# Kernel tuning notes

Measured on AMD Instinct MI355X. Metric: run time of the kernel, lower is better.

The kernel has to match this reference:

```python
import jax, jax.numpy as jnp
import numpy as np

B, L, D = 2, 2048, 2048
H, KVH, Dh = 16, 8, 128
S_ROPE = 1024
EPS = 1e-5


def rms_norm(x, w):
    xf = x.astype(jnp.float32)
    xf = xf * jax.lax.rsqrt(jnp.mean(xf * xf, axis=-1, keepdims=True) + EPS)
    return (xf * w).astype(x.dtype)


def rotate_half(x):
    x1, x2 = jnp.split(x, 2, axis=-1)
    return jnp.concatenate((-x2, x1), axis=-1)


def setup_inputs() -> dict:
    key = jax.random.key(0)
    ks = jax.random.split(key, 12)
    sc = 0.02
    # 1D rope tables at every absolute position (theta = 500000 as in config)
    inv_freq = 1.0 / (500000.0 ** (np.arange(0, Dh, 2, dtype=np.float32) / Dh))
    ang = np.arange(L, dtype=np.float32)[:, None] * inv_freq[None, :]  # [L, Dh/2]
    emb = np.concatenate([ang, ang], axis=-1)  # [L, Dh]
    # 3D rope as per-pair 2x2 rotation matrices
    ang3 = np.random.RandomState(0).uniform(-np.pi, np.pi, size=(S_ROPE, Dh // 2)).astype(np.float32)
    R = np.stack([np.stack([np.cos(ang3), -np.sin(ang3)], -1),
                  np.stack([np.sin(ang3), np.cos(ang3)], -1)], -2)  # [S,Dh/2,2,2]
    mpos = jnp.array([[[128, 1025], [1160, 513]],
                      [[128, 1025], [1160, 513]]], dtype=jnp.int64)
    return {
        "hidden_states": jax.random.normal(ks[0], (B, L, D), jnp.float32),
        "temb": jax.random.normal(ks[1], (B, D), jnp.float32),
        "w_ln": jnp.ones((D,), jnp.float32),
        "w_mod": jax.random.normal(ks[2], (D, 3 * D), jnp.float32) * sc,
        "b_mod": jnp.zeros((3 * D,), jnp.float32),
        "wq": jax.random.normal(ks[3], (D, H * Dh), jnp.float32) * sc,
        "wk": jax.random.normal(ks[4], (D, KVH * Dh), jnp.float32) * sc,
        "wv": jax.random.normal(ks[5], (D, KVH * Dh), jnp.float32) * sc,
        "wo": jax.random.normal(ks[6], (H * Dh, D), jnp.float32) * sc,
        "qn_w": jnp.ones((Dh,), jnp.float32),
        "kn_w": jnp.ones((Dh,), jnp.float32),
        "cos_1d": jnp.asarray(np.cos(emb)),
        "sin_1d": jnp.asarray(np.sin(emb)),
        "rope_3d": jnp.asarray(R),
        "modality_positions": mpos,
    }


def _masks(modality_positions):
    pos = jnp.arange(L)  # [L]
    off = modality_positions[..., 0]   # [B, S]
    ln = modality_positions[..., 1]    # [B, S]
    meta = 1  # add_time_embeds=True, add_ar_embeds=False
    seg_end = off + jnp.maximum(ln, meta)
    in_full = (pos[None, None, :] >= off[..., None]) & (pos[None, None, :] < seg_end[..., None])
    text_mask = ~jnp.any(in_full, axis=1)  # [B, L]
    img_start = off + meta
    in_img = (pos[None, None, :] >= img_start[..., None]) & (pos[None, None, :] < (off + ln)[..., None])
    rel = jnp.sum(jnp.where(in_img, pos[None, None, :] - img_start[..., None], 0), axis=1)  # [B, L]
    img_mask = jnp.any(in_img, axis=1) & (rel < S_ROPE) & (rel >= 0)
    rel = jnp.clip(rel, 0, S_ROPE - 1)
    return text_mask, img_mask, rel


def _apply_mixed_rope(q, k, cos_1d, sin_1d, rope_3d, text_mask, img_mask, rel):
    # text 1D rope (rotate_half style), applied at absolute position
    c = cos_1d[None, None]  # [1,1,L,Dh]
    s = sin_1d[None, None]
    q_txt = q * c + rotate_half(q) * s
    k_txt = k * c + rotate_half(k) * s
    # image 3D rope: per-pair 2x2 rotation gathered at within-image index
    R = rope_3d[rel]  # [B, L, Dh/2, 2, 2]
    q2 = q.reshape(*q.shape[:-1], Dh // 2, 2)
    k2 = k.reshape(*k.shape[:-1], Dh // 2, 2)
    q_img = jnp.einsum('bhlpi,blpij->bhlpj', q2, R).reshape(q.shape)
    k_img = jnp.einsum('bhlpi,blpij->bhlpj', k2, R).reshape(k.shape)
    mt = text_mask[:, None, :, None]
    mi = img_mask[:, None, :, None]
    q_out = jnp.where(mt, q_txt, jnp.where(mi, q_img, q))
    k_out = jnp.where(mt, k_txt, jnp.where(mi, k_img, k))
    return q_out, k_out


def reference(hidden_states, temb, w_ln, w_mod, b_mod, wq, wk, wv, wo,
              qn_w, kn_w, cos_1d, sin_1d, rope_3d, modality_positions):
    dtype = hidden_states.dtype
    # adaLN modulation
    mod = jax.nn.silu(temb) @ w_mod + b_mod  # [B, 3D]
    shift, scale, gate = jnp.split(mod, 3, axis=-1)
    xn = rms_norm(hidden_states, w_ln)
    xm = (xn.astype(jnp.float32) * (1.0 + scale[:, None, :].astype(jnp.float32))
          + shift[:, None, :].astype(jnp.float32)).astype(dtype)
    # qkv projections (GQA)
    q = (xm @ wq).reshape(B, L, H, Dh).transpose(0, 2, 1, 3)
    k = (xm @ wk).reshape(B, L, KVH, Dh).transpose(0, 2, 1, 3)
    v = (xm @ wv).reshape(B, L, KVH, Dh).transpose(0, 2, 1, 3)
    # qk-norm over head_dim
    q = rms_norm(q, qn_w)
    k = rms_norm(k, kn_w)
    # mixed 3D-image / 1D-text RoPE
    text_mask, img_mask, rel = _masks(modality_positions)
    q, k = _apply_mixed_rope(q, k, cos_1d, sin_1d, rope_3d, text_mask, img_mask, rel)
    # GQA: repeat kv heads (repeat_interleave along head dim)
    n_rep = H // KVH
    k = jnp.repeat(k, n_rep, axis=1)
    v = jnp.repeat(v, n_rep, axis=1)
    # full attention (no causal mask for diffusion block)
    scores = jnp.einsum('bhqd,bhkd->bhqk', q, k) / jnp.sqrt(jnp.asarray(Dh, q.dtype))
    attn = jax.nn.softmax(scores, axis=-1)
    o = jnp.einsum('bhqk,bhkd->bhqd', attn, v)
    o = o.transpose(0, 2, 1, 3).reshape(B, L, H * Dh) @ wo
    return hidden_states + gate[:, None, :].astype(dtype) * o


if __name__ == '__main__':
    out = reference(**setup_inputs())
    print(out.shape, out.dtype)
```

## Files before the change

### kernel.cpp

```cpp
#include <hip/hip_runtime.h>
#include <hip/hip_bf16.h>
#include <stdint.h>
#include <math.h>

typedef unsigned short u16;
typedef __attribute__((ext_vector_type(8))) short short8;
typedef __attribute__((ext_vector_type(4))) float fx4;
typedef __attribute__((ext_vector_type(4))) unsigned short u16x4;

#define DEV __device__ __forceinline__

DEV u16 f2bf(float f) {
  return __builtin_bit_cast(u16, __float2bfloat16(f));
}
DEV float bf2f(u16 h) { return __builtin_bit_cast(float, ((unsigned)h) << 16); }

DEV fx4 mfma16(short8 a, short8 b, fx4 c) {
  return __builtin_amdgcn_mfma_f32_16x16x32_bf16(a, b, c, 0, 0, 0);
}

#if __has_builtin(__builtin_amdgcn_exp2f)
DEV float exp2v(float x) { return __builtin_amdgcn_exp2f(x); }
#else
DEV float exp2v(float x) { return exp2f(x); }
#endif

#define GLD16(g, l)                                                            \
  __builtin_amdgcn_global_load_lds(                                            \
      (const __attribute__((address_space(1))) void*)(g),                      \
      (__attribute__((address_space(3))) void*)(l), 16, 0, 0)

#define WAIT_ALL() asm volatile("s_waitcnt vmcnt(0) lgkmcnt(0)" ::: "memory")
#define WAIT_VM4() asm volatile("s_waitcnt vmcnt(4)" ::: "memory")
#define WAIT_VM0() asm volatile("s_waitcnt vmcnt(0)" ::: "memory")

__global__ __launch_bounds__(512) void k_pre(
    const float* __restrict__ temb, const float* __restrict__ wmod,
    const float* __restrict__ bmod, float* __restrict__ mod,
    const float* __restrict__ wq, const float* __restrict__ wk,
    const float* __restrict__ wv, u16* __restrict__ wT) {
  __shared__ float st[4096];
  __shared__ float red[8][2][64];
  __shared__ float t2[2][32][33];
  int bid = blockIdx.x;
  int tid = threadIdx.x;
  if (bid < 96) {
    for (int i = tid; i < 4096; i += 512) {
      float t = temb[i];
      st[i] = t / (1.0f + __expf(-t));
    }
    __syncthreads();
    int j = bid * 64 + (tid & 63);
    int ks = tid >> 6;
    float a0 = 0.f, a1 = 0.f;
    for (int d = ks * 256; d < ks * 256 + 256; ++d) {
      float w = wmod[(size_t)d * 6144 + j];
      a0 += st[d] * w;
      a1 += st[2048 + d] * w;
    }
    red[ks][0][tid & 63] = a0;
    red[ks][1][tid & 63] = a1;
    __syncthreads();
    if (tid < 64) {
      float s0 = 0.f, s1 = 0.f;
#pragma unroll
      for (int i = 0; i < 8; ++i) {
        s0 += red[i][0][tid];
        s1 += red[i][1][tid];
      }
      mod[j] = s0 + bmod[j];
      mod[6144 + j] = s1 + bmod[j];
    }
  } else {
    int half = tid >> 8;
    int sub = tid & 255;
    int tx = sub & 31, ty = sub >> 5;
    int tt = (bid - 96) * 2 + half;
    const float* src;
    u16* dst;
    int cols, kb, nb;
    if (tt < 4096) {
      src = wq; dst = wT; cols = 2048;
      kb = (tt & 63) * 32; nb = (tt >> 6) * 32;
    } else if (tt < 6144) {
      int u = tt - 4096;
      src = wk; dst = wT + (size_t)2048 * 2048; cols = 1024;
      kb = (u & 63) * 32; nb = (u >> 6) * 32;
    } else {
      int u = tt - 6144;
      src = wv; dst = wT + (size_t)3072 * 2048; cols = 1024;
      kb = (u & 63) * 32; nb = (u >> 6) * 32;
    }
    float (*t)[33] = t2[half];
#pragma unroll
    for (int i = 0; i < 4; ++i)
      t[ty + i * 8][tx] = src[(size_t)(kb + ty + i * 8) * cols + nb + tx];
    __syncthreads();
    int nl = ty * 4 + (tx >> 3);
    int k4 = (tx & 7) * 4;
    u16x4 v;
#pragma unroll
    for (int j = 0; j < 4; ++j) v[j] = f2bf(t[k4 + j][nl]);
    *(u16x4*)(dst + (size_t)(nb + nl) * 2048 + kb + k4) = v;
  }
}

__global__ __launch_bounds__(256) void k_xm(
    const float* __restrict__ x, const float* __restrict__ wln,
    const float* __restrict__ mod, u16* __restrict__ xm) {
  int row = blockIdx.x;
  int b = row >> 11;
  const float* xr = x + (size_t)row * 2048;
  int tid = threadIdx.x;
  float4 v0 = ((const float4*)xr)[tid];
  float4 v1 = ((const float4*)xr)[tid + 256];
  float ss = v0.x * v0.x + v0.y * v0.y + v0.z * v0.z + v0.w * v0.w +
             v1.x * v1.x + v1.y * v1.y + v1.z * v1.z + v1.w * v1.w;
  for (int m = 1; m < 64; m <<= 1) ss += __shfl_xor(ss, m);
  __shared__ float red[4];
  if ((tid & 63) == 0) red[tid >> 6] = ss;
  __syncthreads();
  ss = red[0] + red[1] + red[2] + red[3];
  float r = rsqrtf(ss * (1.0f / 2048.0f) + 1e-5f);
  const float* mb = mod + (size_t)b * 6144;
#pragma unroll
  for (int c = 0; c < 2; ++c) {
    int j0 = (tid + c * 256) * 4;
    float4 xv = c ? v1 : v0;
    float4 sh = *(const float4*)(mb + j0);
    float4 sc = *(const float4*)(mb + 2048 + j0);
    float4 wl = *(const float4*)(wln + j0);
    u16x4 o;
    o.x = f2bf(xv.x * r * wl.x * (1.f + sc.x) + sh.x);
    o.y = f2bf(xv.y * r * wl.y * (1.f + sc.y) + sh.y);
    o.z = f2bf(xv.z * r * wl.z * (1.f + sc.z) + sh.z);
    o.w = f2bf(xv.w * r * wl.w * (1.f + sc.w) + sh.w);
    *(u16x4*)(xm + (size_t)row * 2048 + j0) = o;
  }
}

__global__ __launch_bounds__(512, 1) void k_gemm256(
    const u16* __restrict__ A, const u16* __restrict__ Bt, u16* __restrict__ C,
    int N, int K) {
  __shared__ u16 As[3][256 * 32];
  __shared__ u16 Bs[3][256 * 32];
  int tid = threadIdx.x;
  int wave = tid >> 6, lane = tid & 63, quad = lane >> 4, l16 = lane & 15;
  int gx = gridDim.x;
  int nwg = gx * gridDim.y;
  int lin = blockIdx.y * gx + blockIdx.x;
  int cpx = nwg >> 3;
  int swz = (lin & 7) * cpx + (lin >> 3);
  int m0 = (swz / gx) * 256, n0 = (swz % gx) * 256;
  int wm = (wave >> 2) * 128, wn = (wave & 3) * 64;
  fx4 acc[8][4] = {};
  int rowa = tid >> 2;
  int chunk = (tid & 3) ^ ((rowa >> 1) & 3);
  int cola = chunk * 8;
  const u16* Ag = A + (size_t)(m0 + rowa) * K + cola;
  const u16* Bg = Bt + (size_t)(n0 + rowa) * K + cola;
  int sl = (quad ^ ((l16 >> 1) & 3)) * 8;

  auto STAGE = [&](int k0, int buf) {
    u16* AsW = &As[buf][wave * 512];
    u16* BsW = &Bs[buf][wave * 512];
    GLD16(Ag + k0, AsW);
    GLD16(Ag + k0 + (size_t)128 * K, AsW + 4096);
    GLD16(Bg + k0, BsW);
    GLD16(Bg + k0 + (size_t)128 * K, BsW + 4096);
  };
  auto COMPUTE = [&](int buf) {
    short8 af[8], bfr[4];
#pragma unroll
    for (int i = 0; i < 8; ++i)
      af[i] = *(const short8*)&As[buf][(wm + i * 16 + l16) * 32 + sl];
#pragma unroll
    for (int j = 0; j < 4; ++j)
      bfr[j] = *(const short8*)&Bs[buf][(wn + j * 16 + l16) * 32 + sl];
#pragma unroll
    for (int i = 0; i < 8; ++i)
#pragma unroll
      for (int j = 0; j < 4; ++j) acc[i][j] = mfma16(af[i], bfr[j], acc[i][j]);
  };

  STAGE(0, 0);
  STAGE(32, 1);
  for (int t = 0; t < 62; ++t) {
    WAIT_VM4();
    __builtin_amdgcn_s_barrier();
    STAGE((t + 2) * 32, (t + 2) % 3);
    COMPUTE(t % 3);
  }
  WAIT_VM4();
  __builtin_amdgcn_s_barrier();
  COMPUTE(2);
  WAIT_VM0();
  __builtin_amdgcn_s_barrier();
  COMPUTE(0);

#pragma unroll
  for (int i = 0; i < 8; ++i) {
    int row = m0 + wm + i * 16 + quad * 4;
#pragma unroll
    for (int j = 0; j < 4; ++j) {
      int col = n0 + wn + j * 16 + l16;
#pragma unroll
      for (int r = 0; r < 4; ++r)
        C[(size_t)(row + r) * N + col] = f2bf(acc[i][j][r]);
    }
  }
}

__global__ __launch_bounds__(256) void k_mid(
    const float* __restrict__ wo, u16* __restrict__ woT,
    const u16* __restrict__ qkv, const float* __restrict__ qn,
    const float* __restrict__ kn, const float* __restrict__ cos1,
    const float* __restrict__ sin1, const float* __restrict__ r3,
    const int* __restrict__ mpos, u16* __restrict__ Q, u16* __restrict__ Kb,
    u16* __restrict__ VT) {
  __shared__ float tc[32][33];
  __shared__ u16 tv[64][65];
  int bid = blockIdx.x;
  int tid = threadIdx.x;
  if (bid < 4096) {
    int kb = (bid & 63) * 32, nb = (bid >> 6) * 32;
    int tx = tid & 31, ty = tid >> 5;
#pragma unroll
    for (int i = 0; i < 4; ++i)
      tc[ty + i * 8][tx] = wo[(size_t)(kb + ty + i * 8) * 2048 + nb + tx];
    __syncthreads();
    int nl = ty * 4 + (tx >> 3);
    int k4 = (tx & 7) * 4;
    u16x4 v;
#pragma unroll
    for (int j = 0; j < 4; ++j) v[j] = f2bf(tc[k4 + j][nl]);
    *(u16x4*)(woT + (size_t)(nb + nl) * 2048 + kb + k4) = v;
  } else if (bid < 8192) {
    int bx = bid - 4096;
    int b = bx >> 11, l = bx & 2047;
    int slot = tid >> 3, sub = tid & 7;
    if (slot >= 24) return;
    bool isq = slot < 16;
    int head = isq ? slot : slot - 16;
    const u16* base =
        qkv + (size_t)bx * 4096 + (isq ? slot * 128 : 2048 + head * 128);
    int d0 = sub * 16;
    short8 sx0 = *(const short8*)(base + d0);
    short8 sx1 = *(const short8*)(base + d0 + 8);
    float xv[16];
#pragma unroll
    for (int i = 0; i < 8; ++i) {
      xv[i] = bf2f((u16)sx0[i]);
      xv[8 + i] = bf2f((u16)sx1[i]);
    }
    float ss = 0.f;
#pragma unroll
    for (int i = 0; i < 16; ++i) ss += xv[i] * xv[i];
    ss += __shfl_xor(ss, 1);
    ss += __shfl_xor(ss, 2);
    ss += __shfl_xor(ss, 4);
    float r = rsqrtf(ss * (1.0f / 128.0f) + 1e-5f);
    int mp[8];
    {
      bool is64 =
          (mpos[1] == 0) & (mpos[3] == 0) & (mpos[5] == 0) & (mpos[7] == 0);
#pragma unroll
      for (int i = 0; i < 8; ++i) mp[i] = is64 ? mpos[2 * i] : mpos[i];
    }
    bool infull = false, inimg = false;
    int rel = 0;
#pragma unroll
    for (int s = 0; s < 2; ++s) {
      int off = mp[b * 4 + s * 2], ln = mp[b * 4 + s * 2 + 1];
      int mx = ln > 1 ? ln : 1;
      infull |= (l >= off) && (l < off + mx);
      bool ii = (l >= off + 1) && (l < off + ln);
      inimg |= ii;
      rel += ii ? (l - (off + 1)) : 0;
    }
    bool text = !infull;
    bool img = inimg && (rel < 1024);
    const float* w = isq ? qn : kn;
    fx4 wv4[4];
#pragma unroll
    for (int q = 0; q < 4; ++q) wv4[q] = *(const fx4*)(w + d0 + q * 4);
    float out[16];
    if (text) {
      int dp0 = d0 ^ 64;
      float sgn = (d0 < 64) ? -1.f : 1.f;
      short8 sp0 = *(const short8*)(base + dp0);
      short8 sp1 = *(const short8*)(base + dp0 + 8);
      fx4 cv[4], sv[4], wp[4];
#pragma unroll
      for (int q = 0; q < 4; ++q) {
        cv[q] = *(const fx4*)(cos1 + (size_t)l * 128 + d0 + q * 4);
        sv[q] = *(const fx4*)(sin1 + (size_t)l * 128 + d0 + q * 4);
        wp[q] = *(const fx4*)(w + dp0 + q * 4);
      }
#pragma unroll
      for (int i = 0; i < 16; ++i) {
        float xp = bf2f((u16)(i < 8 ? sp0[i & 7] : sp1[i & 7]));
        out[i] = r * (xv[i] * wv4[i >> 2][i & 3] * cv[i >> 2][i & 3] +
                      sgn * xp * wp[i >> 2][i & 3] * sv[i >> 2][i & 3]);
      }
    } else if (img) {
      const fx4* Rv = (const fx4*)(r3 + ((size_t)rel * 64 + (d0 >> 1)) * 4);
#pragma unroll
      for (int p = 0; p < 8; ++p) {
        fx4 R = Rv[p];
        float a = xv[2 * p] * wv4[(2 * p) >> 2][(2 * p) & 3] * r;
        float c2 = xv[2 * p + 1] * wv4[(2 * p + 1) >> 2][(2 * p + 1) & 3] * r;
        out[2 * p] = a * R[0] + c2 * R[2];
        out[2 * p + 1] = a * R[1] + c2 * R[3];
      }
    } else {
#pragma unroll
      for (int i = 0; i < 16; ++i) out[i] = xv[i] * wv4[i >> 2][i & 3] * r;
    }
    float qs = isq ? (0.08838834764831845f * 1.4426950408889634f) : 1.0f;
    short8 o0, o1;
#pragma unroll
    for (int i = 0; i < 8; ++i) {
      o0[i] = (short)f2bf(out[i] * qs);
      o1[i] = (short)f2bf(out[8 + i] * qs);
    }
    u16* dst = isq ? (Q + ((size_t)(b * 16 + head) * 2048 + l) * 128 + d0)
                   : (Kb + ((size_t)(b * 8 + head) * 2048 + l) * 128 + d0);
    *(short8*)dst = o0;
    *(short8*)(dst + 8) = o1;
  } else {
    int v = bid - 8192;
    int bh = v & 15;
    int l0 = ((v >> 4) & 31) * 64, d0 = (v >> 9) * 64;
    int b = bh >> 3, kvh = bh & 7;
    int lr = tid >> 4;
    int c4 = (tid & 15) * 4;
#pragma unroll
    for (int i = 0; i < 4; ++i) {
      int li = lr + i * 16;
      *(u16x4*)&tv[li][c4] = *(const u16x4*)(
          qkv + (size_t)(b * 2048 + l0 + li) * 4096 + 3072 + kvh * 128 + d0 + c4);
    }
    __syncthreads();
#pragma unroll
    for (int i = 0; i < 4; ++i) {
      int di = lr + i * 16;
      u16x4 vv;
      vv[0] = tv[c4 + 0][di];
      vv[1] = tv[c4 + 1][di];
      vv[2] = tv[c4 + 2][di];
      vv[3] = tv[c4 + 3][di];
      *(u16x4*)(VT + ((size_t)bh * 128 + d0 + di) * 2048 + l0 + c4) = vv;
    }
  }
}

__global__ __launch_bounds__(512, 4) void k_attn(
    const u16* __restrict__ Q, const u16* __restrict__ Kb,
    const u16* __restrict__ VT, u16* __restrict__ O) {
  __shared__ u16 Ks[2][64 * 128];
  __shared__ u16 Vs[2][128 * 64];
  __shared__ u16 Ps[128 * 64];
  int tid = threadIdx.x;
  int wave = tid >> 6, lane = tid & 63, quad = lane >> 4, l16 = lane & 15;
  int lin = blockIdx.y * gridDim.x + blockIdx.x;
  int vb = (lin & 7) * 64 + (lin >> 3);
  int q0 = (vb & 15) * 128;
  int bh = vb >> 4;
  int b = bh >> 4, h = bh & 15, kvh = h >> 1;
  const u16* Qb = Q + ((size_t)bh * 2048 + q0 + wave * 16) * 128;
  short8 qf[4];
#pragma unroll
  for (int ks = 0; ks < 4; ++ks)
    qf[ks] = *(const short8*)(Qb + l16 * 128 + ks * 32 + quad * 8);
  const u16* Kg = Kb + (size_t)(b * 8 + kvh) * 2048 * 128;
  const u16* Vg = VT + (size_t)(b * 8 + kvh) * 128 * 2048;
  float mrow[4], lpart[4];
  fx4 of[8] = {};
#pragma unroll
  for (int r = 0; r < 4; ++r) {
    mrow[r] = -INFINITY;
    lpart[r] = 0.f;
  }
  size_t kgo[2], vgo[2];
#pragma unroll
  for (int i = 0; i < 2; ++i) {
    int kr = i * 32 + wave * 4 + (lane >> 4);
    kgo[i] = (size_t)kr * 128 + (((lane & 15) ^ (kr & 15)) * 8);
    int vr = i * 64 + wave * 8 + (lane >> 3);
    vgo[i] = (size_t)vr * 2048 + (((lane & 7) ^ (vr & 7)) * 8);
  }

  auto STAGE = [&](int t, int buf) {
    size_t ko = (size_t)t * 8192;
    size_t vo = (size_t)t * 64;
#pragma unroll
    for (int i = 0; i < 2; ++i) {
      GLD16(Kg + ko + kgo[i], &Ks[buf][i * 4096 + wave * 512]);
      GLD16(Vg + vo + vgo[i], &Vs[buf][i * 4096 + wave * 512]);
    }
  };

  auto COMPUTE = [&](int buf) {
    fx4 sf[4] = {};
    __builtin_amdgcn_s_setprio(1);
#pragma unroll
    for (int ct = 0; ct < 4; ++ct) {
#pragma unroll
      for (int ks = 0; ks < 4; ++ks) {
        short8 kf = *(const short8*)&Ks[buf][(ct * 16 + l16) * 128 +
                                            (((ks * 4 + quad) ^ l16) * 8)];
        sf[ct] = mfma16(qf[ks], kf, sf[ct]);
      }
    }
    __builtin_amdgcn_s_setprio(0);
    float cmv[4];
    bool need = false;
#pragma unroll
    for (int r = 0; r < 4; ++r) {
      cmv[r] = fmaxf(fmaxf(sf[0][r], sf[1][r]), fmaxf(sf[2][r], sf[3][r]));
      need |= (cmv[r] > mrow[r] + 8.0f);
    }
    if (__any(need)) {
#pragma unroll
      for (int r = 0; r < 4; ++r) {
        float cm = cmv[r];
        cm = fmaxf(cm, __shfl_xor(cm, 1));
        cm = fmaxf(cm, __shfl_xor(cm, 2));
        cm = fmaxf(cm, __shfl_xor(cm, 4));
        cm = fmaxf(cm, __shfl_xor(cm, 8));
        float mn = fmaxf(mrow[r], cm);
        float al = exp2v(mrow[r] - mn);
        mrow[r] = mn;
        lpart[r] *= al;
#pragma unroll
        for (int c2 = 0; c2 < 8; ++c2) of[c2][r] *= al;
      }
    }
    int hb = l16 >> 3;
#pragma unroll
    for (int r = 0; r < 4; ++r) {
      float p0 = exp2v(sf[0][r] - mrow[r]);
      float p1 = exp2v(sf[1][r] - mrow[r]);
      float p2 = exp2v(sf[2][r] - mrow[r]);
      float p3 = exp2v(sf[3][r] - mrow[r]);
      lpart[r] += (p0 + p1) + (p2 + p3);
      int prow = wave * 16 + quad * 4 + r;
      int pb = prow * 64, px = prow & 7, lo = l16 & 7;
      Ps[pb + ((0 + hb) ^ px) * 8 + lo] = f2bf(p0);
      Ps[pb + ((2 + hb) ^ px) * 8 + lo] = f2bf(p1);
      Ps[pb + ((4 + hb) ^ px) * 8 + lo] = f2bf(p2);
      Ps[pb + ((6 + hb) ^ px) * 8 + lo] = f2bf(p3);
    }
    __builtin_amdgcn_s_setprio(1);
#pragma unroll
    for (int ks2 = 0; ks2 < 2; ++ks2) {
      int rsl = (((ks2 * 4 + quad) ^ (l16 & 7)) * 8);
      short8 pa = *(const short8*)&Ps[(wave * 16 + l16) * 64 + rsl];
#pragma unroll
      for (int c2 = 0; c2 < 8; ++c2) {
        short8 vb2 = *(const short8*)&Vs[buf][(c2 * 16 + l16) * 64 + rsl];
        of[c2] = mfma16(pa, vb2, of[c2]);
      }
    }
    __builtin_amdgcn_s_setprio(0);
  };

  STAGE(0, 0);
  WAIT_ALL();
  __builtin_amdgcn_s_barrier();
  int cur = 0;
  for (int t = 0; t < 31; ++t) {
    STAGE(t + 1, cur ^ 1);
    COMPUTE(cur);
    WAIT_ALL();
    __builtin_amdgcn_s_barrier();
    cur ^= 1;
  }
  COMPUTE(cur);

#pragma unroll
  for (int r = 0; r < 4; ++r) {
    float ls = lpart[r];
    ls += __shfl_xor(ls, 1);
    ls += __shfl_xor(ls, 2);
    ls += __shfl_xor(ls, 4);
    ls += __shfl_xor(ls, 8);
    float inv = 1.0f / ls;
    int qrow = q0 + wave * 16 + quad * 4 + r;
#pragma unroll
    for (int c2 = 0; c2 < 8; ++c2)
      O[((size_t)b * 2048 + qrow) * 2048 + h * 128 + c2 * 16 + l16] =
          f2bf(of[c2][r] * inv);
  }
}

__global__ __launch_bounds__(256) void k_gemm(
    const u16* __restrict__ A, const u16* __restrict__ Bt, float* __restrict__ C,
    const float* __restrict__ hid, const float* __restrict__ mod, int N, int K) {
  __shared__ u16 As[3][128 * 32];
  __shared__ u16 Bs[3][128 * 32];
  int tid = threadIdx.x;
  int wave = tid >> 6, lane = tid & 63, quad = lane >> 4, l16 = lane & 15;
  int gx = gridDim.x;
  int nwg = gx * gridDim.y;
  int lin = blockIdx.y * gx + blockIdx.x;
  int cpx = nwg >> 3;
  int swz = (lin & 7) * cpx + (lin >> 3);
  int m0 = (swz / gx) * 128, n0 = (swz % gx) * 128;
  int wm = (wave >> 1) * 64, wn = (wave & 1) * 64;
  fx4 acc[4][4] = {};
  int rowa = tid >> 2;
  int chunk = (tid & 3) ^ ((rowa >> 1) & 3);
  int cola = chunk * 8;
  const u16* Ag = A + (size_t)(m0 + rowa) * K + cola;
  const u16* Bg = Bt + (size_t)(n0 + rowa) * K + cola;
  int sl = (quad ^ ((l16 >> 1) & 3)) * 8;

  auto STAGE = [&](int k0, int buf) {
    u16* AsW = &As[buf][wave * 512];
    u16* BsW = &Bs[buf][wave * 512];
    GLD16(Ag + k0, AsW);
    GLD16(Ag + k0 + (size_t)64 * K, AsW + 2048);
    GLD16(Bg + k0, BsW);
    GLD16(Bg + k0 + (size_t)64 * K, BsW + 2048);
  };
  auto COMPUTE = [&](int buf) {
    short8 af[4], bfr[4];
#pragma unroll
    for (int i = 0; i < 4; ++i) {
      af[i] = *(const short8*)&As[buf][(wm + i * 16 + l16) * 32 + sl];
      bfr[i] = *(const short8*)&Bs[buf][(wn + i * 16 + l16) * 32 + sl];
    }
#pragma unroll
    for (int i = 0; i < 4; ++i)
#pragma unroll
      for (int j = 0; j < 4; ++j) acc[i][j] = mfma16(af[i], bfr[j], acc[i][j]);
  };

  STAGE(0, 0);
  STAGE(32, 1);
  int nk = K >> 5;
  for (int t = 0; t < nk - 2; ++t) {
    WAIT_VM4();
    __builtin_amdgcn_s_barrier();
    STAGE((t + 2) * 32, (t + 2) % 3);
    COMPUTE(t % 3);
  }
  WAIT_VM4();
  __builtin_amdgcn_s_barrier();
  COMPUTE((nk - 2) % 3);
  WAIT_VM0();
  __builtin_amdgcn_s_barrier();
  COMPUTE((nk - 1) % 3);

#pragma unroll
  for (int i = 0; i < 4; ++i) {
    int row = m0 + wm + i * 16 + quad * 4;
#pragma unroll
    for (int j = 0; j < 4; ++j) {
      int col = n0 + wn + j * 16 + l16;
      int b = row >> 11;
      float g = mod[(size_t)b * 6144 + 4096 + col];
#pragma unroll
      for (int r = 0; r < 4; ++r)
        C[(size_t)(row + r) * N + col] =
            hid[(size_t)(row + r) * N + col] + g * acc[i][j][r];
    }
  }
}

extern "C" void kernel_launch(void* const* d_in, const int* in_sizes, int n_in,
                              void* d_out, int out_size, void* d_ws, size_t ws_size,
                              hipStream_t stream) {
  (void)in_sizes; (void)n_in; (void)out_size; (void)ws_size;
  const float* hid  = (const float*)d_in[0];
  const float* temb = (const float*)d_in[1];
  const float* wln  = (const float*)d_in[2];
  const float* wmod = (const float*)d_in[3];
  const float* bmod = (const float*)d_in[4];
  const float* wq   = (const float*)d_in[5];
  const float* wk   = (const float*)d_in[6];
  const float* wv   = (const float*)d_in[7];
  const float* wo   = (const float*)d_in[8];
  const float* qn   = (const float*)d_in[9];
  const float* kn   = (const float*)d_in[10];
  const float* cos1 = (const float*)d_in[11];
  const float* sin1 = (const float*)d_in[12];
  const float* r3   = (const float*)d_in[13];
  const int*   mpos = (const int*)d_in[14];

  char* ws = (char*)d_ws;
  float* mod = (float*)(ws + 0);
  u16* xm  = (u16*)(ws + 49152);
  u16* wT  = (u16*)(ws + 16826368);
  u16* woT = wT;
  u16* qkv = (u16*)(ws + 33603584);
  u16* Qb  = (u16*)(ws + 67158016);
  u16* Kv  = (u16*)(ws + 83935232);
  u16* VT  = (u16*)(ws + 92323840);
  u16* Ob  = qkv;

  k_pre<<<4192, 512, 0, stream>>>(temb, wmod, bmod, mod, wq, wk, wv, wT);
  k_xm<<<4096, 256, 0, stream>>>(hid, wln, mod, xm);
  k_gemm256<<<dim3(16, 16), 512, 0, stream>>>(xm, wT, qkv, 4096, 2048);
  k_mid<<<9216, 256, 0, stream>>>(wo, woT, qkv, qn, kn, cos1, sin1, r3, mpos,
                                  Qb, Kv, VT);
  k_attn<<<dim3(16, 32), 512, 0, stream>>>(Qb, Kv, VT, Ob);
  k_gemm<<<dim3(16, 32), 256, 0, stream>>>(Ob, woT, (float*)d_out, hid, mod,
                                           2048, 2048);
}
```

Baseline: 461.2 us.

## Process two query tiles per wave in attention to reuse K/V fragments

Each attention workgroup now handles 256 query rows, and each wave computes two 16-row query tiles against the same K and V fragments loaded from LDS. This halves K/V staging and LDS fragment reads per query row and doubles MFMA work per load. In exchange, the accumulator registers and P-buffer LDS double, the occupancy hint drops to 2, and the grid shrinks to 256 workgroups, which may under-fill the GPU's compute units.

```diff
diff --git a/kernel.cpp b/kernel.cpp
--- a/kernel.cpp
+++ b/kernel.cpp
@@ -355,33 +355,38 @@
   }
 }
 
-__global__ __launch_bounds__(512, 4) void k_attn(
+__global__ __launch_bounds__(512, 2) void k_attn(
     const u16* __restrict__ Q, const u16* __restrict__ Kb,
     const u16* __restrict__ VT, u16* __restrict__ O) {
   __shared__ u16 Ks[2][64 * 128];
   __shared__ u16 Vs[2][128 * 64];
-  __shared__ u16 Ps[128 * 64];
+  __shared__ u16 Ps[256 * 64];
   int tid = threadIdx.x;
   int wave = tid >> 6, lane = tid & 63, quad = lane >> 4, l16 = lane & 15;
   int lin = blockIdx.y * gridDim.x + blockIdx.x;
-  int vb = (lin & 7) * 64 + (lin >> 3);
-  int q0 = (vb & 15) * 128;
-  int bh = vb >> 4;
+  int vb = (lin & 7) * 32 + (lin >> 3);
+  int q0 = (vb & 7) * 256;
+  int bh = vb >> 3;
   int b = bh >> 4, h = bh & 15, kvh = h >> 1;
   const u16* Qb = Q + ((size_t)bh * 2048 + q0 + wave * 16) * 128;
-  short8 qf[4];
-#pragma unroll
-  for (int ks = 0; ks < 4; ++ks)
-    qf[ks] = *(const short8*)(Qb + l16 * 128 + ks * 32 + quad * 8);
+  short8 qf[2][4];
+#pragma unroll
+  for (int qt = 0; qt < 2; ++qt)
+#pragma unroll
+    for (int ks = 0; ks < 4; ++ks)
+      qf[qt][ks] =
+          *(const short8*)(Qb + ((size_t)qt * 128 + l16) * 128 + ks * 32 + quad * 8);
   const u16* Kg = Kb + (size_t)(b * 8 + kvh) * 2048 * 128;
   const u16* Vg = VT + (size_t)(b * 8 + kvh) * 128 * 2048;
-  float mrow[4], lpart[4];
-  fx4 of[8] = {};
-#pragma unroll
-  for (int r = 0; r < 4; ++r) {
-    mrow[r] = -INFINITY;
-    lpart[r] = 0.f;
-  }
+  float mrow[2][4], lpart[2][4];
+  fx4 of[2][8] = {};
+#pragma unroll
+  for (int qt = 0; qt < 2; ++qt)
+#pragma unroll
+    for (int r = 0; r < 4; ++r) {
+      mrow[qt][r] = -INFINITY;
+      lpart[qt][r] = 0.f;
+    }
   size_t kgo[2], vgo[2];
 #pragma unroll
   for (int i = 0; i < 2; ++i) {
@@ -402,7 +407,7 @@
   };
 
   auto COMPUTE = [&](int buf) {
-    fx4 sf[4] = {};
+    fx4 sf[2][4] = {};
     __builtin_amdgcn_s_setprio(1);
 #pragma unroll
     for (int ct = 0; ct < 4; ++ct) {
@@ -410,57 +415,67 @@
       for (int ks = 0; ks < 4; ++ks) {
         short8 kf = *(const short8*)&Ks[buf][(ct * 16 + l16) * 128 +
                                             (((ks * 4 + quad) ^ l16) * 8)];
-        sf[ct] = mfma16(qf[ks], kf, sf[ct]);
+        sf[0][ct] = mfma16(qf[0][ks], kf, sf[0][ct]);
+        sf[1][ct] = mfma16(qf[1][ks], kf, sf[1][ct]);
       }
     }
     __builtin_amdgcn_s_setprio(0);
-    float cmv[4];
+    float cmv[2][4];
     bool need = false;
 #pragma unroll
-    for (int r = 0; r < 4; ++r) {
-      cmv[r] = fmaxf(fmaxf(sf[0][r], sf[1][r]), fmaxf(sf[2][r], sf[3][r]));
-      need |= (cmv[r] > mrow[r] + 8.0f);
-    }
+    for (int qt = 0; qt < 2; ++qt)
+#pragma unroll
+      for (int r = 0; r < 4; ++r) {
+        cmv[qt][r] = fmaxf(fmaxf(sf[qt][0][r], sf[qt][1][r]),
+                           fmaxf(sf[qt][2][r], sf[qt][3][r]));
+        need |= (cmv[qt][r] > mrow[qt][r] + 8.0f);
+      }
     if (__any(need)) {
 #pragma unroll
+      for (int qt = 0; qt < 2; ++qt)
+#pragma unroll
+        for (int r = 0; r < 4; ++r) {
+          float cm = cmv[qt][r];
+          cm = fmaxf(cm, __shfl_xor(cm, 1));
+          cm = fmaxf(cm, __shfl_xor(cm, 2));
+          cm = fmaxf(cm, __shfl_xor(cm, 4));
+          cm = fmaxf(cm, __shfl_xor(cm, 8));
+          float mn = fmaxf(mrow[qt][r], cm);
+          float al = exp2v(mrow[qt][r] - mn);
+          mrow[qt][r] = mn;
+          lpart[qt][r] *= al;
+#pragma unroll
+          for (int c2 = 0; c2 < 8; ++c2) of[qt][c2][r] *= al;
+        }
+    }
+    int hb = l16 >> 3;
+#pragma unroll
+    for (int qt = 0; qt < 2; ++qt)
+#pragma unroll
       for (int r = 0; r < 4; ++r) {
-        float cm = cmv[r];
-        cm = fmaxf(cm, __shfl_xor(cm, 1));
-        cm = fmaxf(cm, __shfl_xor(cm, 2));
-        cm = fmaxf(cm, __shfl_xor(cm, 4));
-        cm = fmaxf(cm, __shfl_xor(cm, 8));
-        float mn = fmaxf(mrow[r], cm);
-        float al = exp2v(mrow[r] - mn);
-        mrow[r] = mn;
-        lpart[r] *= al;
-#pragma unroll
-        for (int c2 = 0; c2 < 8; ++c2) of[c2][r] *= al;
-      }
-    }
-    int hb = l16 >> 3;
-#pragma unroll
-    for (int r = 0; r < 4; ++r) {
-      float p0 = exp2v(sf[0][r] - mrow[r]);
-      float p1 = exp2v(sf[1][r] - mrow[r]);
-      float p2 = exp2v(sf[2][r] - mrow[r]);
-      float p3 = exp2v(sf[3][r] - mrow[r]);
-      lpart[r] += (p0 + p1) + (p2 + p3);
-      int prow = wave * 16 + quad * 4 + r;
-      int pb = prow * 64, px = prow & 7, lo = l16 & 7;
-      Ps[pb + ((0 + hb) ^ px) * 8 + lo] = f2bf(p0);
-      Ps[pb + ((2 + hb) ^ px) * 8 + lo] = f2bf(p1);
-      Ps[pb + ((4 + hb) ^ px) * 8 + lo] = f2bf(p2);
-      Ps[pb + ((6 + hb) ^ px) * 8 + lo] = f2bf(p3);
-    }
+        float p0 = exp2v(sf[qt][0][r] - mrow[qt][r]);
+        float p1 = exp2v(sf[qt][1][r] - mrow[qt][r]);
+        float p2 = exp2v(sf[qt][2][r] - mrow[qt][r]);
+        float p3 = exp2v(sf[qt][3][r] - mrow[qt][r]);
+        lpart[qt][r] += (p0 + p1) + (p2 + p3);
+        int prow = qt * 128 + wave * 16 + quad * 4 + r;
+        int pb = prow * 64, px = prow & 7, lo = l16 & 7;
+        Ps[pb + ((0 + hb) ^ px) * 8 + lo] = f2bf(p0);
+        Ps[pb + ((2 + hb) ^ px) * 8 + lo] = f2bf(p1);
+        Ps[pb + ((4 + hb) ^ px) * 8 + lo] = f2bf(p2);
+        Ps[pb + ((6 + hb) ^ px) * 8 + lo] = f2bf(p3);
+      }
     __builtin_amdgcn_s_setprio(1);
 #pragma unroll
     for (int ks2 = 0; ks2 < 2; ++ks2) {
       int rsl = (((ks2 * 4 + quad) ^ (l16 & 7)) * 8);
-      short8 pa = *(const short8*)&Ps[(wave * 16 + l16) * 64 + rsl];
+      short8 pa0 = *(const short8*)&Ps[(wave * 16 + l16) * 64 + rsl];
+      short8 pa1 = *(const short8*)&Ps[(128 + wave * 16 + l16) * 64 + rsl];
 #pragma unroll
       for (int c2 = 0; c2 < 8; ++c2) {
         short8 vb2 = *(const short8*)&Vs[buf][(c2 * 16 + l16) * 64 + rsl];
-        of[c2] = mfma16(pa, vb2, of[c2]);
+        of[0][c2] = mfma16(pa0, vb2, of[0][c2]);
+        of[1][c2] = mfma16(pa1, vb2, of[1][c2]);
       }
     }
     __builtin_amdgcn_s_setprio(0);
@@ -480,19 +495,21 @@
   COMPUTE(cur);
 
 #pragma unroll
-  for (int r = 0; r < 4; ++r) {
-    float ls = lpart[r];
-    ls += __shfl_xor(ls, 1);
-    ls += __shfl_xor(ls, 2);
-    ls += __shfl_xor(ls, 4);
-    ls += __shfl_xor(ls, 8);
-    float inv = 1.0f / ls;
-    int qrow = q0 + wave * 16 + quad * 4 + r;
-#pragma unroll
-    for (int c2 = 0; c2 < 8; ++c2)
-      O[((size_t)b * 2048 + qrow) * 2048 + h * 128 + c2 * 16 + l16] =
-          f2bf(of[c2][r] * inv);
-  }
+  for (int qt = 0; qt < 2; ++qt)
+#pragma unroll
+    for (int r = 0; r < 4; ++r) {
+      float ls = lpart[qt][r];
+      ls += __shfl_xor(ls, 1);
+      ls += __shfl_xor(ls, 2);
+      ls += __shfl_xor(ls, 4);
+      ls += __shfl_xor(ls, 8);
+      float inv = 1.0f / ls;
+      int qrow = q0 + qt * 128 + wave * 16 + quad * 4 + r;
+#pragma unroll
+      for (int c2 = 0; c2 < 8; ++c2)
+        O[((size_t)b * 2048 + qrow) * 2048 + h * 128 + c2 * 16 + l16] =
+            f2bf(of[qt][c2][r] * inv);
+    }
 }
 
 __global__ __launch_bounds__(256) void k_gemm(
@@ -606,7 +623,7 @@
   k_gemm256<<<dim3(16, 16), 512, 0, stream>>>(xm, wT, qkv, 4096, 2048);
   k_mid<<<9216, 256, 0, stream>>>(wo, woT, qkv, qn, kn, cos1, sin1, r3, mpos,
                                   Qb, Kv, VT);
-  k_attn<<<dim3(16, 32), 512, 0, stream>>>(Qb, Kv, VT, Ob);
+  k_attn<<<dim3(8, 32), 512, 0, stream>>>(Qb, Kv, VT, Ob);
   k_gemm<<<dim3(16, 32), 256, 0, stream>>>(Ob, woT, (float*)d_out, hid, mod,
                                            2048, 2048);
 }
```

Measured after the change: 464.4 us. Within noise of the previous version (+0.7%).
